# Kernel tuning notes

Measured on AMD Instinct MI355X. Metric: run time of the kernel, lower is better.

The kernel has to match this reference:

```python
import jax, jax.numpy as jnp
import numpy as np

NUM_HEADS = 32
NUM_KV_HEADS = 8
HEAD_DIM = 64


def rotate_half(x):
    x1, x2 = jnp.split(x, 2, axis=-1)
    return jnp.concatenate((-x2, x1), axis=-1)


def setup_inputs() -> dict:
    key = jax.random.key(0)
    ks = jax.random.split(key, 7)
    B, S, H = 2, 2048, 2048
    hidden_states = jax.random.normal(ks[0], (B, S, H), dtype=jnp.float32)
    # RoPE angles: build realistic cos/sin from inv_freq for positions 0..S-1
    inv_freq = 1.0 / (10000.0 ** (np.arange(0, HEAD_DIM, 2, dtype=np.float32) / HEAD_DIM))
    t = np.arange(S, dtype=np.float32)
    freqs = np.outer(t, inv_freq)  # [S, HEAD_DIM/2]
    emb = np.concatenate([freqs, freqs], axis=-1)  # [S, HEAD_DIM]
    cos = jnp.broadcast_to(jnp.cos(emb)[None], (B, S, HEAD_DIM)).astype(jnp.float32)
    sin = jnp.broadcast_to(jnp.sin(emb)[None], (B, S, HEAD_DIM)).astype(jnp.float32)
    scale = 1.0 / np.sqrt(H)
    Wq = jax.random.normal(ks[1], (NUM_HEADS * HEAD_DIM, H), dtype=jnp.float32) * scale
    Wk = jax.random.normal(ks[2], (NUM_KV_HEADS * HEAD_DIM, H), dtype=jnp.float32) * scale
    Wv = jax.random.normal(ks[3], (NUM_KV_HEADS * HEAD_DIM, H), dtype=jnp.float32) * scale
    Wo = jax.random.normal(ks[4], (H, H), dtype=jnp.float32) * scale
    return {"hidden_states": hidden_states, "cos": cos, "sin": sin,
            "Wq": Wq, "Wk": Wk, "Wv": Wv, "Wo": Wo}


def reference(hidden_states, cos, sin, Wq, Wk, Wv, Wo):
    B, S, H = hidden_states.shape
    hd = HEAD_DIM
    # QKV projections (torch Linear: y = x @ W.T)
    q = jnp.einsum('bsi,oi->bso', hidden_states, Wq).reshape(B, S, NUM_HEADS, hd).transpose(0, 2, 1, 3)
    k = jnp.einsum('bsi,oi->bso', hidden_states, Wk).reshape(B, S, NUM_KV_HEADS, hd).transpose(0, 2, 1, 3)
    v = jnp.einsum('bsi,oi->bso', hidden_states, Wv).reshape(B, S, NUM_KV_HEADS, hd).transpose(0, 2, 1, 3)
    # RoPE: cos/sin [B,S,hd] -> [B,1,S,hd] broadcast over heads
    c = cos[:, None, :, :]
    s = sin[:, None, :, :]
    q = q * c + rotate_half(q) * s
    k = k * c + rotate_half(k) * s
    # GQA: repeat kv heads to match query heads
    groups = NUM_HEADS // NUM_KV_HEADS
    k = jnp.repeat(k, groups, axis=1)
    v = jnp.repeat(v, groups, axis=1)
    scaling = hd ** -0.5
    scores = jnp.einsum('bhqd,bhkd->bhqk', q, k) * scaling
    causal = jnp.tril(jnp.ones((S, S), dtype=bool))
    scores = jnp.where(causal, scores, jnp.finfo(scores.dtype).min)
    attn = jax.nn.softmax(scores, axis=-1)
    y = jnp.einsum('bhqk,bhkd->bhqd', attn, v)
    y = y.transpose(0, 2, 1, 3).reshape(B, S, H)
    return jnp.einsum('bsi,oi->bso', y, Wo)
```

## Files before the change

kernel.cpp:

```cpp
#include <hip/hip_runtime.h>

typedef __bf16 bf16_t;
typedef bf16_t bf16x8 __attribute__((ext_vector_type(8)));
typedef bf16_t bf16x4 __attribute__((ext_vector_type(4)));
typedef float f32x4 __attribute__((ext_vector_type(4)));
typedef float f32x16 __attribute__((ext_vector_type(16)));

#define MFMA16(a, b, c) __builtin_amdgcn_mfma_f32_16x16x32_bf16(a, b, c, 0, 0, 0)
#define MFMA32(a, b, c) __builtin_amdgcn_mfma_f32_32x32x16_bf16(a, b, c, 0, 0, 0)

#define GLOAD16(gsrc, ldst)                                            \
  __builtin_amdgcn_global_load_lds(                                    \
      (const __attribute__((address_space(1))) void*)(gsrc),           \
      (__attribute__((address_space(3))) void*)(ldst), 16, 0, 0)

constexpr int B_ = 2, S_ = 2048, H_ = 2048, NH = 32, NKV = 8, HD = 64;
constexpr int NQKV = NH * HD + 2 * NKV * HD;
constexpr int M_ROWS = B_ * S_;
constexpr float QSCALE = 0.125f * 1.4426950408889634f;

__global__ __launch_bounds__(256) void cvt_kernel(const float* __restrict__ in,
                                                  bf16_t* __restrict__ out, int n8) {
  int i = blockIdx.x * 256 + threadIdx.x;
  if (i >= n8) return;
  const float4* p = (const float4*)(in + (size_t)i * 8);
  float4 a = p[0], b = p[1];
  bf16x8 o;
  o[0] = (bf16_t)a.x; o[1] = (bf16_t)a.y; o[2] = (bf16_t)a.z; o[3] = (bf16_t)a.w;
  o[4] = (bf16_t)b.x; o[5] = (bf16_t)b.y; o[6] = (bf16_t)b.z; o[7] = (bf16_t)b.w;
  *(bf16x8*)(out + (size_t)i * 8) = o;
}

__global__ __launch_bounds__(256) void cvt3_kernel(const float* __restrict__ s0,
                                                   const float* __restrict__ s1,
                                                   const float* __restrict__ s2,
                                                   bf16_t* __restrict__ out) {
  int i = blockIdx.x * 256 + threadIdx.x;
  const float* src;
  long off;
  if (i < 524288) { src = s0; off = i; }
  else if (i < 655360) { src = s1; off = i - 524288; }
  else { src = s2; off = i - 655360; }
  const float4* p = (const float4*)(src + off * 8);
  float4 a = p[0], b = p[1];
  bf16x8 o;
  o[0] = (bf16_t)a.x; o[1] = (bf16_t)a.y; o[2] = (bf16_t)a.z; o[3] = (bf16_t)a.w;
  o[4] = (bf16_t)b.x; o[5] = (bf16_t)b.y; o[6] = (bf16_t)b.z; o[7] = (bf16_t)b.w;
  *(bf16x8*)(out + (size_t)i * 8) = o;
}

template <bool OUT_BF16>
__global__ __launch_bounds__(256) void gemm_bt(const bf16_t* __restrict__ A,
                                               const bf16_t* __restrict__ Bm,
                                               float* __restrict__ Cf,
                                               bf16_t* __restrict__ Cb,
                                               int M, int N, int K) {
  __shared__ __align__(16) bf16_t As[2][128 * 32];
  __shared__ __align__(16) bf16_t Bs[2][128 * 32];
  const int t = threadIdx.x;
  const int lane = t & 63, w = t >> 6;
  const int l15 = lane & 15, l4 = lane >> 4;
  const int wm = w >> 1, wn = w & 1;
  const long Ar0 = (long)blockIdx.y * 128;
  const long Br0 = (long)blockIdx.x * 128;
  const int nt = K >> 5;

  const int scol = ((lane & 3) ^ ((lane >> 3) & 3)) * 8;
  const int srow = lane >> 2;
  auto stage = [&](int kt, int buf) {
#pragma unroll
    for (int c = 0; c < 2; ++c) {
      const int i = w * 2 + c;
      const bf16_t* gA = A + (Ar0 + i * 16 + srow) * (long)K + kt * 32 + scol;
      const bf16_t* gB = Bm + (Br0 + i * 16 + srow) * (long)K + kt * 32 + scol;
      GLOAD16(gA, &As[buf][i * 512]);
      GLOAD16(gB, &Bs[buf][i * 512]);
    }
  };

  f32x4 acc[4][4] = {};
  stage(0, 0);
  __syncthreads();
  int cur = 0;
  const int rsw = l4 ^ ((l15 >> 1) & 3);
  for (int kt = 0; kt < nt; ++kt) {
    if (kt + 1 < nt) stage(kt + 1, cur ^ 1);
    bf16x8 af[4], bfr[4];
#pragma unroll
    for (int mf = 0; mf < 4; ++mf)
      af[mf] = *(const bf16x8*)&As[cur][(wm * 64 + mf * 16 + l15) * 32 + rsw * 8];
#pragma unroll
    for (int nf = 0; nf < 4; ++nf)
      bfr[nf] = *(const bf16x8*)&Bs[cur][(wn * 64 + nf * 16 + l15) * 32 + rsw * 8];
#pragma unroll
    for (int mf = 0; mf < 4; ++mf)
#pragma unroll
      for (int nf = 0; nf < 4; ++nf)
        acc[mf][nf] = MFMA16(af[mf], bfr[nf], acc[mf][nf]);
    __syncthreads();
    cur ^= 1;
  }
#pragma unroll
  for (int mf = 0; mf < 4; ++mf)
#pragma unroll
    for (int nf = 0; nf < 4; ++nf)
#pragma unroll
      for (int r = 0; r < 4; ++r) {
        long row = Ar0 + wm * 64 + mf * 16 + l4 * 4 + r;
        long col = Br0 + wn * 64 + nf * 16 + l15;
        float v = acc[mf][nf][r];
        if (OUT_BF16)
          Cb[row * N + col] = (bf16_t)v;
        else
          Cf[row * N + col] = v;
      }
}

__global__ __launch_bounds__(256) void rope_kernel(bf16_t* __restrict__ qkv,
                                                   const float* __restrict__ cosb,
                                                   const float* __restrict__ sinb) {
  const int head = blockIdx.y;
  const int i = blockIdx.x * 256 + threadIdx.x;
  const long bs = i >> 2;
  const int d0 = (i & 3) * 8;
  const long base = bs * NQKV + (head < 32 ? head * 64 : 2048 + (head - 32) * 64) + d0;
  const float scl = head < 32 ? QSCALE : 1.0f;
  bf16x8 x1 = *(bf16x8*)(qkv + base);
  bf16x8 x2 = *(bf16x8*)(qkv + base + 32);
  const float4* cp = (const float4*)(cosb + bs * 64 + d0);
  const float4* sp = (const float4*)(sinb + bs * 64 + d0);
  const float4 c0 = cp[0], c1 = cp[1];
  const float4 s0 = sp[0], s1 = sp[1];
  const float cc[8] = {c0.x, c0.y, c0.z, c0.w, c1.x, c1.y, c1.z, c1.w};
  const float ss[8] = {s0.x, s0.y, s0.z, s0.w, s1.x, s1.y, s1.z, s1.w};
  bf16x8 y1, y2;
#pragma unroll
  for (int e = 0; e < 8; ++e) {
    const float f1 = (float)x1[e], f2 = (float)x2[e];
    y1[e] = (bf16_t)((f1 * cc[e] - f2 * ss[e]) * scl);
    y2[e] = (bf16_t)((f2 * cc[e] + f1 * ss[e]) * scl);
  }
  *(bf16x8*)(qkv + base) = y1;
  *(bf16x8*)(qkv + base + 32) = y2;
}

__global__ __launch_bounds__(256) void v_transpose(const bf16_t* __restrict__ qkv,
                                                   bf16_t* __restrict__ vT) {
  __shared__ __align__(16) bf16_t lds[64 * 64];
  const int b = blockIdx.z, kvh = blockIdx.y, s0 = blockIdx.x * 64;
  const int t = threadIdx.x;
  auto key = [](int s) { return (((s & 7) ^ ((s >> 3) & 7)) << 3); };
  const int si = t >> 3, j8 = (t & 7) * 8;
  const bf16_t* src = qkv + ((long)(b * S_ + s0 + si)) * NQKV + 2560 + kvh * 64 + j8;
  *(bf16x8*)&lds[si * 64 + (j8 ^ key(si))] = *(const bf16x8*)src;
  *(bf16x8*)&lds[(si + 32) * 64 + (j8 ^ key(si + 32))] =
      *(const bf16x8*)(src + 32L * NQKV);
  __syncthreads();
  const int d = t >> 2, sg = (t & 3) * 16;
  bf16x8 o0, o1;
#pragma unroll
  for (int e = 0; e < 8; ++e) {
    o0[e] = lds[(sg + e) * 64 + (d ^ key(sg + e))];
    o1[e] = lds[(sg + 8 + e) * 64 + (d ^ key(sg + 8 + e))];
  }
  bf16_t* dst = vT + ((long)(b * NKV + kvh) * 64 + d) * S_ + s0 + sg;
  *(bf16x8*)dst = o0;
  *(bf16x8*)(dst + 8) = o1;
}

__device__ __forceinline__ unsigned pkbf16(float lo, float hi) {
  union { bf16_t h[2]; unsigned u; } x;
  x.h[0] = (bf16_t)lo;
  x.h[1] = (bf16_t)hi;
  return x.u;
}

__global__ __launch_bounds__(128) void attn32_kernel(const bf16_t* __restrict__ qkv,
                                                     const bf16_t* __restrict__ vT,
                                                     bf16_t* __restrict__ y) {
  constexpr int LSTR = 72;
  const int h = blockIdx.y;
  const int b = blockIdx.z;
  const int kvh = h >> 2;
  const int t = threadIdx.x, lane = t & 63, w = t >> 6;
  const int l31 = lane & 31, hd = lane >> 5;
  const long bS = (long)b * S_;

  __shared__ __align__(16) bf16_t Klds[2][64 * LSTR];
  __shared__ __align__(16) bf16_t Vlds[2][64 * LSTR];

  const bf16_t* kbase = qkv + bS * NQKV + NH * HD + kvh * 64;
  const bf16_t* vbase = vT + ((long)(b * NKV + kvh)) * 64 * S_;

  const int row0 = t >> 3, slot = t & 7;
  int woff[4];
#pragma unroll
  for (int c = 0; c < 4; ++c) woff[c] = (row0 + 16 * c) * LSTR + slot * 8;
  int roff[4][2];
#pragma unroll
  for (int ks = 0; ks < 4; ++ks)
#pragma unroll
    for (int kb = 0; kb < 2; ++kb)
      roff[ks][kb] = (kb * 32 + l31) * LSTR + (2 * ks + hd) * 8;

  const bf16_t* kp0[4];
  const bf16_t* vp0[4];
#pragma unroll
  for (int c = 0; c < 4; ++c) {
    kp0[c] = kbase + (long)(row0 + 16 * c) * NQKV + slot * 8;
    vp0[c] = vbase + (long)(row0 + 16 * c) * S_ + slot * 8;
  }

  bf16x8 kreg[4], vreg[4];

  for (int half = 0; half < 2; ++half) {
    const int qt = half ? (int)blockIdx.x : 31 - (int)blockIdx.x;
    const int q0w = qt * 64 + w * 32;
    const int myq = q0w + l31;
    const int NT = qt + 1;

    const bf16_t* qp = qkv + (bS + myq) * NQKV + h * 64 + hd * 8;
    bf16x8 qf[4];
#pragma unroll
    for (int ks = 0; ks < 4; ++ks) qf[ks] = *(const bf16x8*)(qp + ks * 16);

    const bf16_t* kp[4];
    const bf16_t* vp[4];
#pragma unroll
    for (int c = 0; c < 4; ++c) { kp[c] = kp0[c]; vp[c] = vp0[c]; }

    auto ldG = [&]() {
#pragma unroll
      for (int c = 0; c < 4; ++c) {
        kreg[c] = *(const bf16x8*)kp[c];
        vreg[c] = *(const bf16x8*)vp[c];
        kp[c] += 64L * NQKV;
        vp[c] += 64;
      }
    };
    auto wrLDS = [&](int buf) {
#pragma unroll
      for (int c = 0; c < 4; ++c) {
        *(bf16x8*)&Klds[buf][woff[c]] = kreg[c];
        *(bf16x8*)&Vlds[buf][woff[c]] = vreg[c];
      }
    };

    f32x16 yac[2] = {};
    float m = -1e30f, l = 0.f;

    ldG();
    wrLDS(0);
    __syncthreads();

    for (int kt = 0; kt < NT; ++kt) {
      const int buf = kt & 1;
      const int kv0 = kt * 64;
      if (kt + 1 < NT) ldG();

      const bf16_t* Kb = &Klds[buf][0];
      const bf16_t* Vb = &Vlds[buf][0];

      f32x16 sac[2] = {};
      __builtin_amdgcn_s_setprio(1);
#pragma unroll
      for (int ks = 0; ks < 4; ++ks)
#pragma unroll
        for (int kb = 0; kb < 2; ++kb)
          sac[kb] = MFMA32(*(const bf16x8*)&Kb[roff[ks][kb]], qf[ks], sac[kb]);
      __builtin_amdgcn_s_setprio(0);
      if (kv0 + 63 > q0w) {
#pragma unroll
        for (int kb = 0; kb < 2; ++kb)
#pragma unroll
          for (int r = 0; r < 16; ++r) {
            const int kv = kv0 + kb * 32 + (r & 3) + 8 * (r >> 2) + 4 * hd;
            if (kv > myq) sac[kb][r] = -3.0e38f;
          }
      }
      float pm4[8], sm4[8];
#pragma unroll
      for (int g = 0; g < 8; ++g) {
        const int kb = g >> 2, r = (g & 3) * 4;
        pm4[g] = fmaxf(fmaxf(sac[kb][r], sac[kb][r + 1]),
                       fmaxf(sac[kb][r + 2], sac[kb][r + 3]));
      }
      float pm = fmaxf(fmaxf(fmaxf(pm4[0], pm4[1]), fmaxf(pm4[2], pm4[3])),
                       fmaxf(fmaxf(pm4[4], pm4[5]), fmaxf(pm4[6], pm4[7])));
      pm = fmaxf(pm, __shfl_xor(pm, 32, 64));
      if (!__all(pm <= m + 8.f)) {
        const float mnew = fmaxf(m, pm);
        const float sc = __builtin_amdgcn_exp2f(m - mnew);
        l *= sc;
        yac[0] *= sc;
        yac[1] *= sc;
        m = mnew;
      }
#pragma unroll
      for (int kb = 0; kb < 2; ++kb)
#pragma unroll
        for (int r = 0; r < 16; ++r)
          sac[kb][r] = __builtin_amdgcn_exp2f(sac[kb][r] - m);
#pragma unroll
      for (int g = 0; g < 8; ++g) {
        const int kb = g >> 2, r = (g & 3) * 4;
        sm4[g] = (sac[kb][r] + sac[kb][r + 1]) + (sac[kb][r + 2] + sac[kb][r + 3]);
      }
      l += ((sm4[0] + sm4[1]) + (sm4[2] + sm4[3])) +
           ((sm4[4] + sm4[5]) + (sm4[6] + sm4[7]));
#pragma unroll
      for (int ks = 0; ks < 4; ++ks) {
        const int kb = ks >> 1;
        const int Bv = 8 * (ks & 1);
        unsigned a0 = pkbf16(sac[kb][Bv + 0], sac[kb][Bv + 1]);
        unsigned b0 = pkbf16(sac[kb][Bv + 4], sac[kb][Bv + 5]);
        unsigned a1 = pkbf16(sac[kb][Bv + 2], sac[kb][Bv + 3]);
        unsigned b1 = pkbf16(sac[kb][Bv + 6], sac[kb][Bv + 7]);
        asm("v_permlane32_swap_b32 %0, %1" : "+v"(a0), "+v"(b0));
        asm("v_permlane32_swap_b32 %0, %1" : "+v"(a1), "+v"(b1));
        union { unsigned u[4]; bf16x8 v; } pu;
        pu.u[0] = a0; pu.u[1] = a1; pu.u[2] = b0; pu.u[3] = b1;
        __builtin_amdgcn_s_setprio(1);
#pragma unroll
        for (int db = 0; db < 2; ++db)
          yac[db] = MFMA32(*(const bf16x8*)&Vb[roff[ks][db]], pu.v, yac[db]);
        __builtin_amdgcn_s_setprio(0);
      }

      if (kt + 1 < NT) wrLDS(buf ^ 1);
      __syncthreads();
    }

    l += __shfl_xor(l, 32, 64);
    const float inv = __builtin_amdgcn_rcpf(l);
    bf16_t* yp = y + (bS + myq) * (long)H_ + h * 64;
#pragma unroll
    for (int db = 0; db < 2; ++db)
#pragma unroll
      for (int g = 0; g < 4; ++g) {
        bf16x4 o;
        o[0] = (bf16_t)(yac[db][4 * g + 0] * inv);
        o[1] = (bf16_t)(yac[db][4 * g + 1] * inv);
        o[2] = (bf16_t)(yac[db][4 * g + 2] * inv);
        o[3] = (bf16_t)(yac[db][4 * g + 3] * inv);
        *(bf16x4*)(yp + db * 32 + 8 * g + 4 * hd) = o;
      }
  }
}

extern "C" void kernel_launch(void* const* d_in, const int* in_sizes, int n_in,
                              void* d_out, int out_size, void* d_ws, size_t ws_size,
                              hipStream_t stream) {
  const float* hs = (const float*)d_in[0];
  const float* cosb = (const float*)d_in[1];
  const float* sinb = (const float*)d_in[2];
  const float* Wq = (const float*)d_in[3];
  const float* Wk = (const float*)d_in[4];
  const float* Wv = (const float*)d_in[5];
  const float* Wo = (const float*)d_in[6];
  float* out = (float*)d_out;

  char* ws = (char*)d_ws;
  bf16_t* hsb  = (bf16_t*)(ws);
  bf16_t* wqkv = (bf16_t*)(ws + 16777216);
  bf16_t* wo   = (bf16_t*)(ws + 29360128);
  bf16_t* qkv  = (bf16_t*)(ws + 37748736);
  bf16_t* vT   = (bf16_t*)(ws + 62914560);
  bf16_t* yb   = (bf16_t*)(ws + 67108864);

  cvt_kernel<<<4096, 256, 0, stream>>>(hs, hsb, 1048576);
  cvt3_kernel<<<3072, 256, 0, stream>>>(Wq, Wk, Wv, wqkv);
  cvt_kernel<<<2048, 256, 0, stream>>>(Wo, wo, 524288);

  gemm_bt<true><<<dim3(24, 32), 256, 0, stream>>>(hsb, wqkv, nullptr, qkv,
                                                  M_ROWS, NQKV, H_);
  rope_kernel<<<dim3(64, 40), 256, 0, stream>>>(qkv, cosb, sinb);
  v_transpose<<<dim3(32, 8, 2), 256, 0, stream>>>(qkv, vT);
  attn32_kernel<<<dim3(16, 32, 2), 128, 0, stream>>>(qkv, vT, yb);
  gemm_bt<false><<<dim3(16, 32), 256, 0, stream>>>(yb, wo, out, nullptr,
                                                   M_ROWS, H_, H_);
}
```

Before: 254.4 us.

## Share K/V tiles across two GQA heads per block and merge conversion kernels

The attention kernel now runs 256 threads per block, with two wave pairs handling two query heads that share the same KV head. Each K/V tile is loaded into LDS once and reused by both heads, which halves global K/V traffic and the per-thread load count. The grid becomes 512 blocks instead of 1024. The three fp32-to-bf16 conversion launches are also merged into one kernel to cut launch overhead. The tradeoff is fewer blocks for load balancing and more waves contending per block at each sync.

```diff
diff --git a/kernel.cpp b/kernel.cpp
--- a/kernel.cpp
+++ b/kernel.cpp
@@ -19,34 +19,34 @@
 constexpr int M_ROWS = B_ * S_;
 constexpr float QSCALE = 0.125f * 1.4426950408889634f;
 
-__global__ __launch_bounds__(256) void cvt_kernel(const float* __restrict__ in,
-                                                  bf16_t* __restrict__ out, int n8) {
-  int i = blockIdx.x * 256 + threadIdx.x;
-  if (i >= n8) return;
-  const float4* p = (const float4*)(in + (size_t)i * 8);
+__global__ __launch_bounds__(256) void cvt_all(const float* __restrict__ hs,
+                                               const float* __restrict__ Wq,
+                                               const float* __restrict__ Wk,
+                                               const float* __restrict__ Wv,
+                                               const float* __restrict__ Wo,
+                                               bf16_t* __restrict__ hsb,
+                                               bf16_t* __restrict__ wqkv,
+                                               bf16_t* __restrict__ wo) {
+  const long i = (long)blockIdx.x * 256 + threadIdx.x;
+  const float* src;
+  bf16_t* dst;
+  if (i < 1048576) {
+    src = hs + i * 8;            dst = hsb + i * 8;
+  } else if (i < 1572864) {
+    const long j = i - 1048576;  src = Wq + j * 8;  dst = wqkv + j * 8;
+  } else if (i < 1703936) {
+    const long j = i - 1572864;  src = Wk + j * 8;  dst = wqkv + 4194304 + j * 8;
+  } else if (i < 1835008) {
+    const long j = i - 1703936;  src = Wv + j * 8;  dst = wqkv + 5242880 + j * 8;
+  } else {
+    const long j = i - 1835008;  src = Wo + j * 8;  dst = wo + j * 8;
+  }
+  const float4* p = (const float4*)src;
   float4 a = p[0], b = p[1];
   bf16x8 o;
   o[0] = (bf16_t)a.x; o[1] = (bf16_t)a.y; o[2] = (bf16_t)a.z; o[3] = (bf16_t)a.w;
   o[4] = (bf16_t)b.x; o[5] = (bf16_t)b.y; o[6] = (bf16_t)b.z; o[7] = (bf16_t)b.w;
-  *(bf16x8*)(out + (size_t)i * 8) = o;
-}
-
-__global__ __launch_bounds__(256) void cvt3_kernel(const float* __restrict__ s0,
-                                                   const float* __restrict__ s1,
-                                                   const float* __restrict__ s2,
-                                                   bf16_t* __restrict__ out) {
-  int i = blockIdx.x * 256 + threadIdx.x;
-  const float* src;
-  long off;
-  if (i < 524288) { src = s0; off = i; }
-  else if (i < 655360) { src = s1; off = i - 524288; }
-  else { src = s2; off = i - 655360; }
-  const float4* p = (const float4*)(src + off * 8);
-  float4 a = p[0], b = p[1];
-  bf16x8 o;
-  o[0] = (bf16_t)a.x; o[1] = (bf16_t)a.y; o[2] = (bf16_t)a.z; o[3] = (bf16_t)a.w;
-  o[4] = (bf16_t)b.x; o[5] = (bf16_t)b.y; o[6] = (bf16_t)b.z; o[7] = (bf16_t)b.w;
-  *(bf16x8*)(out + (size_t)i * 8) = o;
+  *(bf16x8*)dst = o;
 }
 
 template <bool OUT_BF16>
@@ -175,15 +175,18 @@
   return x.u;
 }
 
-__global__ __launch_bounds__(128) void attn32_kernel(const bf16_t* __restrict__ qkv,
-                                                     const bf16_t* __restrict__ vT,
-                                                     bf16_t* __restrict__ y) {
+__global__ __launch_bounds__(256, 4) void attn32_kernel(const bf16_t* __restrict__ qkv,
+                                                        const bf16_t* __restrict__ vT,
+                                                        bf16_t* __restrict__ y) {
   constexpr int LSTR = 72;
-  const int h = blockIdx.y;
-  const int b = blockIdx.z;
-  const int kvh = h >> 2;
+  const int bx = blockIdx.x;
+  const int p = bx & 15;
+  const int hp = (bx >> 4) & 1;
+  const int kvh = (bx >> 5) & 7;
+  const int b = bx >> 8;
   const int t = threadIdx.x, lane = t & 63, w = t >> 6;
   const int l31 = lane & 31, hd = lane >> 5;
+  const int h = kvh * 4 + hp * 2 + (w >> 1);
   const long bS = (long)b * S_;
 
   __shared__ __align__(16) bf16_t Klds[2][64 * LSTR];
@@ -193,9 +196,9 @@
   const bf16_t* vbase = vT + ((long)(b * NKV + kvh)) * 64 * S_;
 
   const int row0 = t >> 3, slot = t & 7;
-  int woff[4];
-#pragma unroll
-  for (int c = 0; c < 4; ++c) woff[c] = (row0 + 16 * c) * LSTR + slot * 8;
+  int woff[2];
+#pragma unroll
+  for (int c = 0; c < 2; ++c) woff[c] = (row0 + 32 * c) * LSTR + slot * 8;
   int roff[4][2];
 #pragma unroll
   for (int ks = 0; ks < 4; ++ks)
@@ -203,19 +206,19 @@
     for (int kb = 0; kb < 2; ++kb)
       roff[ks][kb] = (kb * 32 + l31) * LSTR + (2 * ks + hd) * 8;
 
-  const bf16_t* kp0[4];
-  const bf16_t* vp0[4];
-#pragma unroll
-  for (int c = 0; c < 4; ++c) {
-    kp0[c] = kbase + (long)(row0 + 16 * c) * NQKV + slot * 8;
-    vp0[c] = vbase + (long)(row0 + 16 * c) * S_ + slot * 8;
-  }
-
-  bf16x8 kreg[4], vreg[4];
+  const bf16_t* kp0[2];
+  const bf16_t* vp0[2];
+#pragma unroll
+  for (int c = 0; c < 2; ++c) {
+    kp0[c] = kbase + (long)(row0 + 32 * c) * NQKV + slot * 8;
+    vp0[c] = vbase + (long)(row0 + 32 * c) * S_ + slot * 8;
+  }
+
+  bf16x8 kreg[2], vreg[2];
 
   for (int half = 0; half < 2; ++half) {
-    const int qt = half ? (int)blockIdx.x : 31 - (int)blockIdx.x;
-    const int q0w = qt * 64 + w * 32;
+    const int qt = half ? p : 31 - p;
+    const int q0w = qt * 64 + (w & 1) * 32;
     const int myq = q0w + l31;
     const int NT = qt + 1;
 
@@ -224,14 +227,14 @@
 #pragma unroll
     for (int ks = 0; ks < 4; ++ks) qf[ks] = *(const bf16x8*)(qp + ks * 16);
 
-    const bf16_t* kp[4];
-    const bf16_t* vp[4];
-#pragma unroll
-    for (int c = 0; c < 4; ++c) { kp[c] = kp0[c]; vp[c] = vp0[c]; }
+    const bf16_t* kp[2];
+    const bf16_t* vp[2];
+#pragma unroll
+    for (int c = 0; c < 2; ++c) { kp[c] = kp0[c]; vp[c] = vp0[c]; }
 
     auto ldG = [&]() {
 #pragma unroll
-      for (int c = 0; c < 4; ++c) {
+      for (int c = 0; c < 2; ++c) {
         kreg[c] = *(const bf16x8*)kp[c];
         vreg[c] = *(const bf16x8*)vp[c];
         kp[c] += 64L * NQKV;
@@ -240,7 +243,7 @@
     };
     auto wrLDS = [&](int buf) {
 #pragma unroll
-      for (int c = 0; c < 4; ++c) {
+      for (int c = 0; c < 2; ++c) {
         *(bf16x8*)&Klds[buf][woff[c]] = kreg[c];
         *(bf16x8*)&Vlds[buf][woff[c]] = vreg[c];
       }
@@ -368,15 +371,13 @@
   bf16_t* vT   = (bf16_t*)(ws + 62914560);
   bf16_t* yb   = (bf16_t*)(ws + 67108864);
 
-  cvt_kernel<<<4096, 256, 0, stream>>>(hs, hsb, 1048576);
-  cvt3_kernel<<<3072, 256, 0, stream>>>(Wq, Wk, Wv, wqkv);
-  cvt_kernel<<<2048, 256, 0, stream>>>(Wo, wo, 524288);
+  cvt_all<<<9216, 256, 0, stream>>>(hs, Wq, Wk, Wv, Wo, hsb, wqkv, wo);
 
   gemm_bt<true><<<dim3(24, 32), 256, 0, stream>>>(hsb, wqkv, nullptr, qkv,
                                                   M_ROWS, NQKV, H_);
   rope_kernel<<<dim3(64, 40), 256, 0, stream>>>(qkv, cosb, sinb);
   v_transpose<<<dim3(32, 8, 2), 256, 0, stream>>>(qkv, vT);
-  attn32_kernel<<<dim3(16, 32, 2), 128, 0, stream>>>(qkv, vT, yb);
+  attn32_kernel<<<512, 256, 0, stream>>>(qkv, vT, yb);
   gemm_bt<false><<<dim3(16, 32), 256, 0, stream>>>(yb, wo, out, nullptr,
                                                    M_ROWS, H_, H_);
 }
```

Result: faster. 206.8 us (-18.7%).
